# Kernel optimization log

Hardware: AMD Instinct MI355X
Metric: run time of the kernel (lower is better)

The kernel has to match this reference:

```python
import jax, jax.numpy as jnp
import numpy as np

B, P, ENC, DEC, ATT, EMB, V, MAXLEN = 64, 196, 2048, 1024, 1024, 1024, 10000, 20


def setup_inputs() -> dict:
    key = jax.random.key(0)
    ks = jax.random.split(key, 20)
    s = 0.02
    inp = {
        'encoder_out': jax.random.normal(ks[0], (B, 14, 14, ENC), jnp.float32),
        'encoded_captions': jax.random.randint(ks[1], (B, MAXLEN), 0, V),
        'caption_lengths': jax.random.randint(ks[2], (B, 1), 2, MAXLEN + 1).at[0, 0].set(MAXLEN),
        # embedding
        'emb_table': jax.random.uniform(ks[3], (V, EMB), jnp.float32, -0.1, 0.1),
        # attention MLP (weight_norm Linear == plain Linear math)
        'We': jax.random.normal(ks[4], (ATT, ENC)) * s,
        'be': jnp.zeros((ATT,), jnp.float32),
        'Wd': jax.random.normal(ks[5], (ATT, DEC)) * s,
        'bd': jnp.zeros((ATT,), jnp.float32),
        'Wf': jax.random.normal(ks[6], (1, ATT)) * s,
        'bf': jnp.zeros((1,), jnp.float32),
        # top_down_attention LSTMCell: input = EMB+ENC+DEC
        'W_ih1': jax.random.normal(ks[7], (4 * DEC, EMB + ENC + DEC)) * s,
        'W_hh1': jax.random.normal(ks[8], (4 * DEC, DEC)) * s,
        'b_ih1': jnp.zeros((4 * DEC,), jnp.float32),
        'b_hh1': jnp.zeros((4 * DEC,), jnp.float32),
        # language_model LSTMCell: input = ENC+DEC
        'W_ih2': jax.random.normal(ks[9], (4 * DEC, ENC + DEC)) * s,
        'W_hh2': jax.random.normal(ks[10], (4 * DEC, DEC)) * s,
        'b_ih2': jnp.zeros((4 * DEC,), jnp.float32),
        'b_hh2': jnp.zeros((4 * DEC,), jnp.float32),
        # output heads
        'Wfc1': jax.random.normal(ks[11], (V, DEC)) * s,
        'bfc1': jnp.zeros((V,), jnp.float32),
        'Wfc': jax.random.uniform(ks[12], (V, DEC), jnp.float32, -0.1, 0.1),
        'bfc': jnp.zeros((V,), jnp.float32),
    }
    return inp


def _lstm_cell(x, h, c, Wih, Whh, bih, bhh):
    g = x @ Wih.T + bih + h @ Whh.T + bhh
    i, f, gg, o = jnp.split(g, 4, axis=-1)  # torch gate order: i, f, g, o
    c2 = jax.nn.sigmoid(f) * c + jax.nn.sigmoid(i) * jnp.tanh(gg)
    h2 = jax.nn.sigmoid(o) * jnp.tanh(c2)
    return h2, c2


def _decode(encoder_out, encoded_captions, caption_lengths, emb_table,
            We, be, Wd, bd, Wf, bf,
            W_ih1, W_hh1, b_ih1, b_hh1, W_ih2, W_hh2, b_ih2, b_hh2,
            Wfc1, bfc1, Wfc, bfc):
    b = encoder_out.shape[0]
    enc = encoder_out.reshape(b, -1, encoder_out.shape[-1])  # (B,P,ENC)
    enc_mean = enc.mean(axis=1)
    cl = caption_lengths.squeeze(1)
    sort_ind = jnp.argsort(-cl)
    cl = cl[sort_ind]
    enc = enc[sort_ind]
    enc_mean = enc_mean[sort_ind]
    caps = encoded_captions[sort_ind]
    dec_len = cl - 1  # (B,)
    embeds = emb_table[caps]  # (B,T,EMB)
    Tdec = caps.shape[1] - 1
    # precompute encoder attention projection (loop-invariant, same math)
    att1 = jnp.einsum('bpe,ae->bpa', enc, We) + be  # (B,P,ATT)

    def step(carry, t):
        h1, c1, h2, c2 = carry
        active = (t < dec_len)[:, None]  # (B,1)
        x1 = jnp.concatenate([h2, enc_mean, embeds[:, t, :]], axis=1)
        h1n, c1n = _lstm_cell(x1, h1, c1, W_ih1, W_hh1, b_ih1, b_hh1)
        h1n = jnp.where(active, h1n, h1)
        c1n = jnp.where(active, c1n, c1)
        # Bahdanau attention
        att2 = h1n @ Wd.T + bd  # (B,ATT)
        e = jnp.einsum('bpa,a->bp', jax.nn.relu(att1 + att2[:, None, :]), Wf[0]) + bf[0]
        alpha = jax.nn.softmax(e, axis=1)
        awe = jnp.einsum('bpe,bp->be', enc, alpha)
        preds1 = h1n @ Wfc1.T + bfc1  # dropout is identity at eval
        x2 = jnp.concatenate([awe, h1n], axis=1)
        h2n, c2n = _lstm_cell(x2, h2, c2, W_ih2, W_hh2, b_ih2, b_hh2)
        h2n = jnp.where(active, h2n, h2)
        c2n = jnp.where(active, c2n, c2)
        preds = h2n @ Wfc.T + bfc
        preds = jnp.where(active, preds, 0.0)
        preds1 = jnp.where(active, preds1, 0.0)
        return (h1n, c1n, h2n, c2n), (preds, preds1)

    z = jnp.zeros((b, DEC), jnp.float32)
    (_, _, _, _), (pr, pr1) = jax.lax.scan(step, (z, z, z, z), jnp.arange(Tdec))
    predictions = jnp.transpose(pr, (1, 0, 2))  # (B,Tdec,V)
    predictions1 = jnp.transpose(pr1, (1, 0, 2))
    return predictions, predictions1, caps, dec_len, sort_ind


def reference(encoder_out, encoded_captions, caption_lengths, emb_table,
              We, be, Wd, bd, Wf, bf,
              W_ih1, W_hh1, b_ih1, b_hh1, W_ih2, W_hh2, b_ih2, b_hh2,
              Wfc1, bfc1, Wfc, bfc):
    return _decode(encoder_out, encoded_captions, caption_lengths, emb_table,
                   We, be, Wd, bd, Wf, bf,
                   W_ih1, W_hh1, b_ih1, b_hh1, W_ih2, W_hh2, b_ih2, b_hh2,
                   Wfc1, bfc1, Wfc, bfc)
```

## Files before the change

### kernel.cpp

```cpp
#include <hip/hip_runtime.h>
#include <cmath>

#define B_ 64
#define P_ 196
#define ENC_ 2048
#define DEC_ 1024
#define V_ 10000
#define MAXLEN_ 20
#define TDEC_ 19

typedef __attribute__((ext_vector_type(8))) short bf16x8;
typedef __attribute__((ext_vector_type(4))) float f32x4;


__device__ __align__(16) short g_encb[(size_t)12544 * 2048];
__device__ __align__(16) short g_encbt[(size_t)12544 * 2048];
__device__ __align__(16) short g_att1[(size_t)12544 * 1024];
__device__ __align__(16) short g_Wp1t[(size_t)4096 * 2048];
__device__ __align__(16) short g_Wemt[(size_t)4096 * 2048];
__device__ __align__(16) short g_Wembt[(size_t)4096 * 1024];
__device__ __align__(16) short g_Wc2t[(size_t)4096 * 4096];
__device__ __align__(16) short g_Webt[(size_t)1024 * 2048];
__device__ __align__(16) short g_Wdt[(size_t)1024 * 1024];
__device__ __align__(16) short g_Wfc1t[(size_t)10000 * 1024];
__device__ __align__(16) short g_Wfct[(size_t)10000 * 1024];
__device__ __align__(16) short g_xs1[(size_t)20 * 64 * 2048];
__device__ __align__(16) short g_xemb[(size_t)19 * 64 * 1024];
__device__ __align__(16) short g_xc2[(size_t)20 * 64 * 4096];
__device__ __align__(16) short g_em[64 * 2048];
__device__ __align__(16) float g_preemb[(size_t)19 * 64 * 4096];
__device__ __align__(16) float g_preem[64 * 4096];
__device__ __align__(16) float g_part[(size_t)16 * 64 * 4096];
__device__ __align__(16) float g_att2p[(size_t)8 * 64 * 1024];
__device__ __align__(16) float g_e[64 * P_];
__device__ __align__(16) float g_c1[64 * 1024];
__device__ __align__(16) float g_c2[64 * 1024];
__device__ int g_ibuf[64 + 64 + 64 * MAXLEN_];

__device__ __forceinline__ short f2b(float f) {
  unsigned u = __float_as_uint(f);
  u += 0x7FFFu + ((u >> 16) & 1u);
  return (short)(u >> 16);
}
__device__ __forceinline__ float b2f(short s) {
  return __uint_as_float(((unsigned)(unsigned short)s) << 16);
}

__global__ void k_sort(const int* __restrict__ cl_in, const int* __restrict__ caps_in,
                       int* __restrict__ sind, int* __restrict__ declen, int* __restrict__ caps_s,
                       float* __restrict__ out_caps, float* __restrict__ out_declen,
                       float* __restrict__ out_sind) {
  int i = threadIdx.x;
  __shared__ int cl[B_];
  cl[i] = cl_in[i];
  __syncthreads();
  int my = cl[i], pos = 0;
  for (int j = 0; j < B_; ++j) {
    int cj = cl[j];
    if (cj > my || (cj == my && j < i)) pos++;
  }
  sind[pos] = i;
  __syncthreads();
  int sb = sind[i];
  int dl = cl[sb] - 1;
  declen[i] = dl;
  out_declen[i] = (float)dl;
  out_sind[i] = (float)sb;
  for (int t = 0; t < MAXLEN_; ++t) {
    int v = caps_in[sb * MAXLEN_ + t];
    caps_s[i * MAXLEN_ + t] = v;
    out_caps[i * MAXLEN_ + t] = (float)v;
  }
}

__global__ __launch_bounds__(256) void k_encprep(const float* __restrict__ enc,
                                                 const int* __restrict__ sind,
                                                 short* __restrict__ encb,
                                                 short* __restrict__ encbt) {
  int mg = blockIdx.x;
  int b = mg / P_, p = mg - b * P_;
  int tid = threadIdx.x;
  const float* src = enc + ((size_t)sind[b] * P_ + p) * ENC_ + tid * 8;
  float4 a = *(const float4*)src;
  float4 c = *(const float4*)(src + 4);
  bf16x8 v;
  v[0] = f2b(a.x); v[1] = f2b(a.y); v[2] = f2b(a.z); v[3] = f2b(a.w);
  v[4] = f2b(c.x); v[5] = f2b(c.y); v[6] = f2b(c.z); v[7] = f2b(c.w);
  *(bf16x8*)(encb + (size_t)mg * ENC_ + tid * 8) = v;
  size_t off = (((size_t)(mg >> 4) * 64 + (tid >> 2)) << 9) +
               (((mg & 15) | ((tid & 3) << 4)) << 3);
  *(bf16x8*)(encbt + off) = v;
}

__global__ __launch_bounds__(64) void k_encmeanb(const short* __restrict__ encb,
                                                 short* __restrict__ em) {
  int b = blockIdx.x;
  int col0 = blockIdx.y * 512 + threadIdx.x * 8;
  const short* src = encb + (size_t)b * P_ * ENC_ + col0;
  float acc[8] = {};
  for (int p = 0; p < P_; ++p) {
    bf16x8 v = *(const bf16x8*)(src + (size_t)p * ENC_);
#pragma unroll
    for (int j = 0; j < 8; ++j) acc[j] += b2f(v[j]);
  }
#pragma unroll
  for (int j = 0; j < 8; ++j) em[b * 2048 + col0 + j] = f2b(acc[j] * (1.0f / 196.0f));
}

__global__ __launch_bounds__(256) void k_prefill(const float* __restrict__ emb,
                                                 const int* __restrict__ caps_s,
                                                 short* __restrict__ xemb) {
  int t = blockIdx.x, b = blockIdx.y, tid = threadIdx.x;
  short* xr = xemb + ((size_t)t * 64 + b) * 1024;
  int cap = caps_s[b * MAXLEN_ + t];
  int j = tid * 4;
  float4 v = *(const float4*)(emb + (size_t)cap * 1024 + j);
  short4 o;
  o.x = f2b(v.x); o.y = f2b(v.y); o.z = f2b(v.z); o.w = f2b(v.w);
  *(short4*)(xr + j) = o;
}

__global__ void k_f2bts(const float* __restrict__ src, int Kstride, int c0, int ncols,
                        short* __restrict__ dst, int Ktot, int koff) {
  int idx = blockIdx.x * 256 + threadIdx.x;
  int kc = ncols >> 3;
  int r = idx / kc, k8 = (idx - r * kc) << 3;
  const float* s = src + (size_t)r * Kstride + c0 + k8;
  float4 a = *(const float4*)s;
  float4 c = *(const float4*)(s + 4);
  bf16x8 v;
  v[0] = f2b(a.x); v[1] = f2b(a.y); v[2] = f2b(a.z); v[3] = f2b(a.w);
  v[4] = f2b(c.x); v[5] = f2b(c.y); v[6] = f2b(c.z); v[7] = f2b(c.w);
  int kg = koff + k8;
  size_t off = (((size_t)(r >> 4) * (Ktot >> 5) + (kg >> 5)) << 9) +
               (((r & 15) | (((kg >> 3) & 3) << 4)) << 3);
  *(bf16x8*)(dst + off) = v;
}

__global__ __launch_bounds__(512) void k_att1_t(const short* __restrict__ At,
                                                const short* __restrict__ Wt,
                                                const float* __restrict__ be,
                                                short* __restrict__ Cb) {
  int wg = blockIdx.x;
  wg = (wg & 7) * 49 + (wg >> 3);
  int bx = wg >> 2, by = wg & 3;
  int wave = threadIdx.x >> 6, lane = threadIdx.x & 63;
  int mt0 = bx * 8 + (wave >> 2) * 4;
  int nt0 = by * 16 + (wave & 3) * 4;
  f32x4 acc[4][4] = {};
  const short* Ab = At + ((size_t)mt0 * 64 << 9) + lane * 8;
  const short* Wb = Wt + ((size_t)nt0 * 64 << 9) + lane * 8;
  for (int kt = 0; kt < 64; ++kt) {
    bf16x8 a[4], b[4];
#pragma unroll
    for (int i = 0; i < 4; ++i) a[i] = *(const bf16x8*)(Ab + (((size_t)i * 64 + kt) << 9));
#pragma unroll
    for (int j = 0; j < 4; ++j) b[j] = *(const bf16x8*)(Wb + (((size_t)j * 64 + kt) << 9));
#pragma unroll
    for (int i = 0; i < 4; ++i)
#pragma unroll
      for (int j = 0; j < 4; ++j)
        acc[i][j] = __builtin_amdgcn_mfma_f32_16x16x32_bf16(a[i], b[j], acc[i][j], 0, 0, 0);
  }
  int rr = (lane >> 4) * 4, cc = lane & 15;
  int m0 = mt0 * 16, n0 = nt0 * 16;
#pragma unroll
  for (int i = 0; i < 4; ++i)
#pragma unroll
    for (int j = 0; j < 4; ++j) {
      int n = n0 + j * 16 + cc;
      float bn = be[n];
#pragma unroll
      for (int r = 0; r < 4; ++r) {
        int m = m0 + i * 16 + rr + r;
        Cb[(size_t)m * 1024 + n] = f2b(acc[i][j][r] + bn);
      }
    }
}

__global__ __launch_bounds__(256) void k_skinny_t(const short* __restrict__ A, int lda,
                                                  const short* __restrict__ Wt, int ldw,
                                                  int N, int kchunk, float* __restrict__ part) {
  int wave = threadIdx.x >> 6, lane = threadIdx.x & 63;
  int n0 = blockIdx.x * 128 + wave * 32;
  int kb = blockIdx.y * kchunk;
  int lr = lane & 15, lk = (lane >> 4) * 8;
  int ntk = ldw >> 5;
  int nt0 = n0 >> 4;
  f32x4 acc[4][2] = {};
  const short* Ab = A + (size_t)lr * lda + kb + lk;
  const short* Wb0 = Wt + (((size_t)nt0 * ntk + (kb >> 5)) << 9) + lane * 8;
  const short* Wb1 = Wt + (((size_t)(nt0 + 1) * ntk + (kb >> 5)) << 9) + lane * 8;
  int nkt = kchunk >> 5;
  for (int kt = 0; kt < nkt; ++kt) {
    bf16x8 a[4], b0, b1;
#pragma unroll
    for (int i = 0; i < 4; ++i) a[i] = *(const bf16x8*)(Ab + (size_t)i * 16 * lda + kt * 32);
    b0 = *(const bf16x8*)(Wb0 + ((size_t)kt << 9));
    b1 = *(const bf16x8*)(Wb1 + ((size_t)kt << 9));
#pragma unroll
    for (int i = 0; i < 4; ++i) {
      acc[i][0] = __builtin_amdgcn_mfma_f32_16x16x32_bf16(a[i], b0, acc[i][0], 0, 0, 0);
      acc[i][1] = __builtin_amdgcn_mfma_f32_16x16x32_bf16(a[i], b1, acc[i][1], 0, 0, 0);
    }
  }
  float* po = part + (size_t)blockIdx.y * 64 * N;
  int rr = (lane >> 4) * 4, cc = lane & 15;
#pragma unroll
  for (int i = 0; i < 4; ++i)
#pragma unroll
    for (int j = 0; j < 2; ++j) {
      int n = n0 + j * 16 + cc;
#pragma unroll
      for (int r = 0; r < 4; ++r) {
        int m = i * 16 + rr + r;
        po[(size_t)m * N + n] = acc[i][j][r];
      }
    }
}

__global__ void k_sumn(const float* __restrict__ part, int nsplit, float* __restrict__ dst) {
  int idx = blockIdx.x * 256 + threadIdx.x;
  float s = 0.0f;
  for (int q = 0; q < nsplit; ++q) s += part[(size_t)q * 64 * 4096 + idx];
  dst[idx] = s;
}

__global__ __launch_bounds__(256) void k_mid_emb4(const short* __restrict__ xemb,
                                                  const short* __restrict__ Wt,
                                                  float* __restrict__ preemb) {
  int wg = blockIdx.x;
  wg = (wg & 7) * 38 + (wg >> 3);
  int t = wg % 19;
  int nch = wg / 19;
  const short* A = xemb + (size_t)t * 64 * 1024;
  int wave = threadIdx.x >> 6, lane = threadIdx.x & 63;
  int nt0 = nch * 16 + wave * 4;
  int lr = lane & 15, lk = (lane >> 4) * 8;
  f32x4 acc[4][4] = {};
  const short* Ab = A + (size_t)lr * 1024 + lk;
  const short* Wb[4];
#pragma unroll
  for (int j = 0; j < 4; ++j) Wb[j] = Wt + ((size_t)(nt0 + j) * 32 << 9) + lane * 8;
  for (int kt = 0; kt < 32; ++kt) {
    bf16x8 a[4], b[4];
#pragma unroll
    for (int j = 0; j < 4; ++j) b[j] = *(const bf16x8*)(Wb[j] + ((size_t)kt << 9));
#pragma unroll
    for (int i = 0; i < 4; ++i) a[i] = *(const bf16x8*)(Ab + (size_t)i * 16 * 1024 + kt * 32);
#pragma unroll
    for (int i = 0; i < 4; ++i)
#pragma unroll
      for (int j = 0; j < 4; ++j)
        acc[i][j] = __builtin_amdgcn_mfma_f32_16x16x32_bf16(a[i], b[j], acc[i][j], 0, 0, 0);
  }
  float* po = preemb + (size_t)t * 64 * 4096;
  int rr = (lane >> 4) * 4, cc = lane & 15;
#pragma unroll
  for (int i = 0; i < 4; ++i)
#pragma unroll
    for (int j = 0; j < 4; ++j) {
      int n = (nt0 + j) * 16 + cc;
#pragma unroll
      for (int r = 0; r < 4; ++r) {
        int m = i * 16 + rr + r;
        po[(size_t)m * 4096 + n] = acc[i][j][r];
      }
    }
}

__global__ void k_gates(const float* __restrict__ part, int nsplit,
                        const float* __restrict__ pre, const float* __restrict__ pre2,
                        const float* __restrict__ bih, const float* __restrict__ bhh,
                        float* __restrict__ c,
                        const short* __restrict__ hold, int ldo,
                        short* __restrict__ dst1, int ld1,
                        short* __restrict__ dst2, int ld2,
                        const int* __restrict__ declen, int t) {
  int idx = blockIdx.x * 256 + threadIdx.x;
  int b = idx >> 10, j = idx & 1023;
  const float* pb = part + (size_t)b * 4096;
  float gi = bih[j] + bhh[j];
  float gf = bih[1024 + j] + bhh[1024 + j];
  float gg = bih[2048 + j] + bhh[2048 + j];
  float go = bih[3072 + j] + bhh[3072 + j];
  if (pre) {
    const float* pp = pre + (size_t)b * 4096;
    gi += pp[j]; gf += pp[j + 1024]; gg += pp[j + 2048]; go += pp[j + 3072];
  }
  if (pre2) {
    const float* pp = pre2 + (size_t)b * 4096;
    gi += pp[j]; gf += pp[j + 1024]; gg += pp[j + 2048]; go += pp[j + 3072];
  }
  for (int s = 0; s < nsplit; ++s) {
    const float* p = pb + (size_t)s * 64 * 4096;
    gi += p[j]; gf += p[j + 1024]; gg += p[j + 2048]; go += p[j + 3072];
  }
  float si = 1.0f / (1.0f + expf(-gi));
  float sf = 1.0f / (1.0f + expf(-gf));
  float so = 1.0f / (1.0f + expf(-go));
  float cn = sf * c[idx] + si * tanhf(gg);
  float hn = so * tanhf(cn);
  short hb;
  if (t < declen[b]) {
    c[idx] = cn;
    hb = f2b(hn);
  } else {
    hb = hold[b * ldo + j];
  }
  dst1[b * ld1 + j] = hb;
  dst2[b * ld2 + j] = hb;
}

__global__ __launch_bounds__(256) void k_e(const short* __restrict__ att1,
                                           const float* __restrict__ att2p,
                                           const float* __restrict__ bd,
                                           const float* __restrict__ Wf,
                                           const float* __restrict__ bf,
                                           float* __restrict__ e) {
  __shared__ float a2[1024];
  int b = blockIdx.x / 49, pq = blockIdx.x % 49;
  for (int i = threadIdx.x; i < 1024; i += 256) {
    float s = bd[i];
#pragma unroll
    for (int q = 0; q < 4; ++q) s += att2p[q * 65536 + b * 1024 + i];
    a2[i] = s;
  }
  __syncthreads();
  int wave = threadIdx.x >> 6, lane = threadIdx.x & 63;
  int p = pq * 4 + wave;
  const short* a1 = att1 + ((size_t)(b * P_ + p)) * 1024;
  float s = 0.0f;
#pragma unroll
  for (int h = 0; h < 2; ++h) {
    int k0 = lane * 8 + h * 512;
    bf16x8 v = *(const bf16x8*)(a1 + k0);
#pragma unroll
    for (int j = 0; j < 8; ++j) s += Wf[k0 + j] * fmaxf(b2f(v[j]) + a2[k0 + j], 0.0f);
  }
#pragma unroll
  for (int off = 32; off; off >>= 1) s += __shfl_down(s, off);
  if (lane == 0) e[b * P_ + p] = s + bf[0];
}

__global__ __launch_bounds__(256) void k_sawe(const float* __restrict__ e,
                                              const short* __restrict__ encb,
                                              short* __restrict__ xc2t) {
  int b = blockIdx.x, ch = blockIdx.y;
  __shared__ float al[P_];
  __shared__ float red[8][256];
  int tid = threadIdx.x;
  if (tid < 64) {
    float vals[4];
    float mx = -1e30f;
#pragma unroll
    for (int q = 0; q < 4; ++q) {
      int p = tid + q * 64;
      vals[q] = (p < P_) ? e[b * P_ + p] : -1e30f;
      mx = fmaxf(mx, vals[q]);
    }
#pragma unroll
    for (int off = 32; off; off >>= 1) mx = fmaxf(mx, __shfl_xor(mx, off));
    float sum = 0.0f;
#pragma unroll
    for (int q = 0; q < 4; ++q) {
      int p = tid + q * 64;
      vals[q] = (p < P_) ? expf(vals[q] - mx) : 0.0f;
      sum += vals[q];
    }
#pragma unroll
    for (int off = 32; off; off >>= 1) sum += __shfl_xor(sum, off);
    float inv = 1.0f / sum;
#pragma unroll
    for (int q = 0; q < 4; ++q) {
      int p = tid + q * 64;
      if (p < P_) al[p] = vals[q] * inv;
    }
  }
  __syncthreads();
  int pg = tid >> 5, cg = tid & 31;
  int col = ch * 256 + cg * 8;
  const short* src = encb + (size_t)b * P_ * ENC_ + col;
  float acc[8] = {};
  for (int p = pg; p < P_; p += 8) {
    bf16x8 v = *(const bf16x8*)(src + (size_t)p * ENC_);
    float ap = al[p];
#pragma unroll
    for (int j = 0; j < 8; ++j) acc[j] += ap * b2f(v[j]);
  }
#pragma unroll
  for (int j = 0; j < 8; ++j) red[pg][cg * 8 + j] = acc[j];
  __syncthreads();
  float s = 0.0f;
#pragma unroll
  for (int g = 0; g < 8; ++g) s += red[g][tid];
  xc2t[b * 4096 + ch * 256 + tid] = f2b(s);
}

__global__ __launch_bounds__(256) void k_head4(const short* __restrict__ Aall,
                                               const short* __restrict__ Wt,
                                               const float* __restrict__ bias,
                                               float* __restrict__ outp,
                                               const int* __restrict__ declen) {
  int wg = blockIdx.x;
  wg = (wg & 7) * 95 + (wg >> 3);
  int t = wg % 19;
  int nch = wg / 19;
  const short* A = Aall + (size_t)t * (64 * 4096);
  int wave = threadIdx.x >> 6, lane = threadIdx.x & 63;
  int nt0 = nch * 16 + wave * 4;
  int lr = lane & 15, lk = (lane >> 4) * 8;
  f32x4 acc[4][4] = {};
  const short* Ab = A + (size_t)lr * 4096 + lk;
  const short* Wb[4];
  bool ok[4];
#pragma unroll
  for (int j = 0; j < 4; ++j) {
    ok[j] = (nt0 + j) < (V_ >> 4);
    Wb[j] = Wt + ((size_t)(ok[j] ? nt0 + j : 0) * 32 << 9) + lane * 8;
  }
  for (int kt = 0; kt < 32; ++kt) {
    bf16x8 a[4], b[4];
#pragma unroll
    for (int j = 0; j < 4; ++j) b[j] = *(const bf16x8*)(Wb[j] + ((size_t)kt << 9));
#pragma unroll
    for (int i = 0; i < 4; ++i) a[i] = *(const bf16x8*)(Ab + (size_t)i * 16 * 4096 + kt * 32);
#pragma unroll
    for (int i = 0; i < 4; ++i)
#pragma unroll
      for (int j = 0; j < 4; ++j)
        acc[i][j] = __builtin_amdgcn_mfma_f32_16x16x32_bf16(a[i], b[j], acc[i][j], 0, 0, 0);
  }
  int rr = (lane >> 4) * 4, cc = lane & 15;
#pragma unroll
  for (int j = 0; j < 4; ++j) {
    if (!ok[j]) continue;
    int n = (nt0 + j) * 16 + cc;
    float bn = bias[n];
#pragma unroll
    for (int i = 0; i < 4; ++i) {
#pragma unroll
      for (int r = 0; r < 4; ++r) {
        int b = i * 16 + rr + r;
        float val = acc[i][j][r] + bn;
        outp[((size_t)b * TDEC_ + t) * V_ + n] = (t < declen[b]) ? val : 0.0f;
      }
    }
  }
}

extern "C" void kernel_launch(void* const* d_in, const int* in_sizes, int n_in,
                              void* d_out, int out_size, void* d_ws, size_t ws_size,
                              hipStream_t stream) {
  (void)in_sizes; (void)n_in; (void)d_ws; (void)ws_size; (void)out_size;
  const float* enc  = (const float*)d_in[0];
  const int*   caps = (const int*)d_in[1];
  const int*   cl   = (const int*)d_in[2];
  const float* emb  = (const float*)d_in[3];
  const float* We   = (const float*)d_in[4];
  const float* be   = (const float*)d_in[5];
  const float* Wd   = (const float*)d_in[6];
  const float* bd   = (const float*)d_in[7];
  const float* Wf   = (const float*)d_in[8];
  const float* bf   = (const float*)d_in[9];
  const float* Wih1 = (const float*)d_in[10];
  const float* Whh1 = (const float*)d_in[11];
  const float* bih1 = (const float*)d_in[12];
  const float* bhh1 = (const float*)d_in[13];
  const float* Wih2 = (const float*)d_in[14];
  const float* Whh2 = (const float*)d_in[15];
  const float* bih2 = (const float*)d_in[16];
  const float* bhh2 = (const float*)d_in[17];
  const float* Wfc1 = (const float*)d_in[18];
  const float* bfc1 = (const float*)d_in[19];
  const float* Wfc  = (const float*)d_in[20];
  const float* bfc  = (const float*)d_in[21];
  float* out = (float*)d_out;

  short *encb, *encbt, *att1, *Wp1t, *Wemt, *Wembt, *Wc2t, *Webt, *Wdt, *Wfc1t, *Wfct;
  short *xs1, *xemb, *xc2, *em;
  float *preemb, *preem, *part, *att2p, *e, *c1, *c2;
  int* ib;
  hipGetSymbolAddress((void**)&encb, HIP_SYMBOL(g_encb));
  hipGetSymbolAddress((void**)&encbt, HIP_SYMBOL(g_encbt));
  hipGetSymbolAddress((void**)&att1, HIP_SYMBOL(g_att1));
  hipGetSymbolAddress((void**)&Wp1t, HIP_SYMBOL(g_Wp1t));
  hipGetSymbolAddress((void**)&Wemt, HIP_SYMBOL(g_Wemt));
  hipGetSymbolAddress((void**)&Wembt, HIP_SYMBOL(g_Wembt));
  hipGetSymbolAddress((void**)&Wc2t, HIP_SYMBOL(g_Wc2t));
  hipGetSymbolAddress((void**)&Webt, HIP_SYMBOL(g_Webt));
  hipGetSymbolAddress((void**)&Wdt, HIP_SYMBOL(g_Wdt));
  hipGetSymbolAddress((void**)&Wfc1t, HIP_SYMBOL(g_Wfc1t));
  hipGetSymbolAddress((void**)&Wfct, HIP_SYMBOL(g_Wfct));
  hipGetSymbolAddress((void**)&xs1, HIP_SYMBOL(g_xs1));
  hipGetSymbolAddress((void**)&xemb, HIP_SYMBOL(g_xemb));
  hipGetSymbolAddress((void**)&xc2, HIP_SYMBOL(g_xc2));
  hipGetSymbolAddress((void**)&em, HIP_SYMBOL(g_em));
  hipGetSymbolAddress((void**)&preemb, HIP_SYMBOL(g_preemb));
  hipGetSymbolAddress((void**)&preem, HIP_SYMBOL(g_preem));
  hipGetSymbolAddress((void**)&part, HIP_SYMBOL(g_part));
  hipGetSymbolAddress((void**)&att2p, HIP_SYMBOL(g_att2p));
  hipGetSymbolAddress((void**)&e, HIP_SYMBOL(g_e));
  hipGetSymbolAddress((void**)&c1, HIP_SYMBOL(g_c1));
  hipGetSymbolAddress((void**)&c2, HIP_SYMBOL(g_c2));
  hipGetSymbolAddress((void**)&ib, HIP_SYMBOL(g_ibuf));
  int* sind = ib;
  int* declen = ib + 64;
  int* caps_s = ib + 128;

  float* out_preds  = out;
  float* out_preds1 = out + (size_t)B_ * TDEC_ * V_;
  float* out_caps   = out + 2ull * B_ * TDEC_ * V_;
  float* out_declen = out_caps + B_ * MAXLEN_;
  float* out_sind   = out_declen + B_;

  k_sort<<<1, 64, 0, stream>>>(cl, caps, sind, declen, caps_s, out_caps, out_declen, out_sind);
  hipMemsetAsync(c1, 0, 64 * 1024 * sizeof(float), stream);
  hipMemsetAsync(c2, 0, 64 * 1024 * sizeof(float), stream);
  hipMemsetAsync(xs1, 0, (size_t)64 * 2048 * sizeof(short), stream);
  hipMemsetAsync(xc2, 0, (size_t)64 * 4096 * sizeof(short), stream);
  k_encprep<<<12544, 256, 0, stream>>>(enc, sind, encb, encbt);
  k_encmeanb<<<dim3(64, 4), 64, 0, stream>>>(encb, em);
  k_prefill<<<dim3(19, 64), 256, 0, stream>>>(emb, caps_s, xemb);
  k_f2bts<<<2048, 256, 0, stream>>>(Wih1, 4096, 0, 1024, Wp1t, 2048, 0);
  k_f2bts<<<2048, 256, 0, stream>>>(Whh1, 1024, 0, 1024, Wp1t, 2048, 1024);
  k_f2bts<<<4096, 256, 0, stream>>>(Wih1, 4096, 1024, 2048, Wemt, 2048, 0);
  k_f2bts<<<2048, 256, 0, stream>>>(Wih1, 4096, 3072, 1024, Wembt, 1024, 0);
  k_f2bts<<<6144, 256, 0, stream>>>(Wih2, 3072, 0, 3072, Wc2t, 4096, 0);
  k_f2bts<<<2048, 256, 0, stream>>>(Whh2, 1024, 0, 1024, Wc2t, 4096, 3072);
  k_f2bts<<<1024, 256, 0, stream>>>(We, 2048, 0, 2048, Webt, 2048, 0);
  k_f2bts<<<512, 256, 0, stream>>>(Wd, 1024, 0, 1024, Wdt, 1024, 0);
  k_f2bts<<<5000, 256, 0, stream>>>(Wfc1, 1024, 0, 1024, Wfc1t, 1024, 0);
  k_f2bts<<<5000, 256, 0, stream>>>(Wfc, 1024, 0, 1024, Wfct, 1024, 0);
  k_att1_t<<<392, 512, 0, stream>>>(encbt, Webt, be, att1);
  k_skinny_t<<<dim3(32, 4), 256, 0, stream>>>(em, 2048, Wemt, 2048, 4096, 512, part);
  k_sumn<<<1024, 256, 0, stream>>>(part, 4, preem);
  k_mid_emb4<<<304, 256, 0, stream>>>(xemb, Wembt, preemb);

  for (int t = 0; t < TDEC_; ++t) {
    short* s1t = xs1 + (size_t)t * 64 * 2048;
    short* s1n = xs1 + (size_t)(t + 1) * 64 * 2048;
    short* x2t = xc2 + (size_t)t * 64 * 4096;
    short* x2n = xc2 + (size_t)(t + 1) * 64 * 4096;
    k_skinny_t<<<dim3(32, 8), 256, 0, stream>>>(s1t, 2048, Wp1t, 2048, 4096, 256, part);
    k_gates<<<256, 256, 0, stream>>>(part, 8, preemb + (size_t)t * 64 * 4096, preem,
                                     bih1, bhh1, c1, s1t + 1024, 2048,
                                     s1n + 1024, 2048, x2t + 2048, 4096, declen, t);
    k_skinny_t<<<dim3(8, 4), 256, 0, stream>>>(x2t + 2048, 4096, Wdt, 1024, 1024, 256, att2p);
    k_e<<<3136, 256, 0, stream>>>(att1, att2p, bd, Wf, bf, e);
    k_sawe<<<dim3(64, 8), 256, 0, stream>>>(e, encb, x2t);
    k_skinny_t<<<dim3(32, 8), 256, 0, stream>>>(x2t, 4096, Wc2t, 4096, 4096, 512, part);
    k_gates<<<256, 256, 0, stream>>>(part, 8, nullptr, nullptr, bih2, bhh2, c2, s1t, 2048,
                                     s1n, 2048, x2n + 3072, 4096, declen, t);
  }
  k_head4<<<760, 256, 0, stream>>>(xc2 + 2048, Wfc1t, bfc1, out_preds1, declen);
  k_head4<<<760, 256, 0, stream>>>(xc2 + 64 * 4096 + 3072, Wfct, bfc, out_preds, declen);
}
```

Measured before the change: 1.833 ms.

## Batch weight conversions into one launch, coarsen attention-score kernel, drop att1 swizzle

Ten separate fp32-to-bf16 weight conversion launches are merged into one kernel that picks its job from a block-offset table passed by value, cutting launch overhead. The per-step attention-score kernel now has each wave handle four pixels, so a block covers 16, which reduces block count and repeats the 1024-element att2 reduction into shared memory fewer times. The att1 GEMM drops its XCD-aware block index swizzle in favour of a plain 2D grid, which may change L2 locality.

```diff
diff --git a/kernel.cpp b/kernel.cpp
--- a/kernel.cpp
+++ b/kernel.cpp
@@ -120,33 +120,46 @@
   *(short4*)(xr + j) = o;
 }
 
-__global__ void k_f2bts(const float* __restrict__ src, int Kstride, int c0, int ncols,
-                        short* __restrict__ dst, int Ktot, int koff) {
-  int idx = blockIdx.x * 256 + threadIdx.x;
-  int kc = ncols >> 3;
+struct F2BJobs {
+  const float* src[10];
+  short* dst[10];
+  int kstride[10];
+  int c0[10];
+  int ncols[10];
+  int ktot[10];
+  int koff[10];
+  int base[11];
+};
+
+__global__ __launch_bounds__(256) void k_f2bt_all(F2BJobs jb) {
+  int bg = blockIdx.x;
+  int j = 0;
+#pragma unroll
+  for (int q = 1; q < 10; ++q)
+    if (bg >= jb.base[q]) j = q;
+  int idx = (bg - jb.base[j]) * 256 + threadIdx.x;
+  int kc = jb.ncols[j] >> 3;
   int r = idx / kc, k8 = (idx - r * kc) << 3;
-  const float* s = src + (size_t)r * Kstride + c0 + k8;
+  const float* s = jb.src[j] + (size_t)r * jb.kstride[j] + jb.c0[j] + k8;
   float4 a = *(const float4*)s;
   float4 c = *(const float4*)(s + 4);
   bf16x8 v;
   v[0] = f2b(a.x); v[1] = f2b(a.y); v[2] = f2b(a.z); v[3] = f2b(a.w);
   v[4] = f2b(c.x); v[5] = f2b(c.y); v[6] = f2b(c.z); v[7] = f2b(c.w);
-  int kg = koff + k8;
+  int kg = jb.koff[j] + k8;
+  int Ktot = jb.ktot[j];
   size_t off = (((size_t)(r >> 4) * (Ktot >> 5) + (kg >> 5)) << 9) +
                (((r & 15) | (((kg >> 3) & 3) << 4)) << 3);
-  *(bf16x8*)(dst + off) = v;
+  *(bf16x8*)(jb.dst[j] + off) = v;
 }
 
 __global__ __launch_bounds__(512) void k_att1_t(const short* __restrict__ At,
                                                 const short* __restrict__ Wt,
                                                 const float* __restrict__ be,
                                                 short* __restrict__ Cb) {
-  int wg = blockIdx.x;
-  wg = (wg & 7) * 49 + (wg >> 3);
-  int bx = wg >> 2, by = wg & 3;
   int wave = threadIdx.x >> 6, lane = threadIdx.x & 63;
-  int mt0 = bx * 8 + (wave >> 2) * 4;
-  int nt0 = by * 16 + (wave & 3) * 4;
+  int mt0 = blockIdx.x * 8 + (wave >> 2) * 4;
+  int nt0 = blockIdx.y * 16 + (wave & 3) * 4;
   f32x4 acc[4][4] = {};
   const short* Ab = At + ((size_t)mt0 * 64 << 9) + lane * 8;
   const short* Wb = Wt + ((size_t)nt0 * 64 << 9) + lane * 8;
@@ -319,7 +332,7 @@
                                            const float* __restrict__ bf,
                                            float* __restrict__ e) {
   __shared__ float a2[1024];
-  int b = blockIdx.x / 49, pq = blockIdx.x % 49;
+  int b = blockIdx.x / 13, pq = blockIdx.x % 13;
   for (int i = threadIdx.x; i < 1024; i += 256) {
     float s = bd[i];
 #pragma unroll
@@ -328,19 +341,23 @@
   }
   __syncthreads();
   int wave = threadIdx.x >> 6, lane = threadIdx.x & 63;
-  int p = pq * 4 + wave;
-  const short* a1 = att1 + ((size_t)(b * P_ + p)) * 1024;
-  float s = 0.0f;
-#pragma unroll
-  for (int h = 0; h < 2; ++h) {
-    int k0 = lane * 8 + h * 512;
-    bf16x8 v = *(const bf16x8*)(a1 + k0);
-#pragma unroll
-    for (int j = 0; j < 8; ++j) s += Wf[k0 + j] * fmaxf(b2f(v[j]) + a2[k0 + j], 0.0f);
-  }
-#pragma unroll
-  for (int off = 32; off; off >>= 1) s += __shfl_down(s, off);
-  if (lane == 0) e[b * P_ + p] = s + bf[0];
+#pragma unroll
+  for (int i = 0; i < 4; ++i) {
+    int p = pq * 16 + wave * 4 + i;
+    if (p >= P_) break;
+    const short* a1 = att1 + ((size_t)(b * P_ + p)) * 1024;
+    float s = 0.0f;
+#pragma unroll
+    for (int h = 0; h < 2; ++h) {
+      int k0 = lane * 8 + h * 512;
+      bf16x8 v = *(const bf16x8*)(a1 + k0);
+#pragma unroll
+      for (int j = 0; j < 8; ++j) s += Wf[k0 + j] * fmaxf(b2f(v[j]) + a2[k0 + j], 0.0f);
+    }
+#pragma unroll
+    for (int off = 32; off; off >>= 1) s += __shfl_down(s, off);
+    if (lane == 0) e[b * P_ + p] = s + bf[0];
+  }
 }
 
 __global__ __launch_bounds__(256) void k_sawe(const float* __restrict__ e,
@@ -522,17 +539,27 @@
   k_encprep<<<12544, 256, 0, stream>>>(enc, sind, encb, encbt);
   k_encmeanb<<<dim3(64, 4), 64, 0, stream>>>(encb, em);
   k_prefill<<<dim3(19, 64), 256, 0, stream>>>(emb, caps_s, xemb);
-  k_f2bts<<<2048, 256, 0, stream>>>(Wih1, 4096, 0, 1024, Wp1t, 2048, 0);
-  k_f2bts<<<2048, 256, 0, stream>>>(Whh1, 1024, 0, 1024, Wp1t, 2048, 1024);
-  k_f2bts<<<4096, 256, 0, stream>>>(Wih1, 4096, 1024, 2048, Wemt, 2048, 0);
-  k_f2bts<<<2048, 256, 0, stream>>>(Wih1, 4096, 3072, 1024, Wembt, 1024, 0);
-  k_f2bts<<<6144, 256, 0, stream>>>(Wih2, 3072, 0, 3072, Wc2t, 4096, 0);
-  k_f2bts<<<2048, 256, 0, stream>>>(Whh2, 1024, 0, 1024, Wc2t, 4096, 3072);
-  k_f2bts<<<1024, 256, 0, stream>>>(We, 2048, 0, 2048, Webt, 2048, 0);
-  k_f2bts<<<512, 256, 0, stream>>>(Wd, 1024, 0, 1024, Wdt, 1024, 0);
-  k_f2bts<<<5000, 256, 0, stream>>>(Wfc1, 1024, 0, 1024, Wfc1t, 1024, 0);
-  k_f2bts<<<5000, 256, 0, stream>>>(Wfc, 1024, 0, 1024, Wfct, 1024, 0);
-  k_att1_t<<<392, 512, 0, stream>>>(encbt, Webt, be, att1);
+  {
+    F2BJobs jb;
+    const float* srcs[10] = {Wih1, Whh1, Wih1, Wih1, Wih2, Whh2, We, Wd, Wfc1, Wfc};
+    short* dsts[10] = {Wp1t, Wp1t, Wemt, Wembt, Wc2t, Wc2t, Webt, Wdt, Wfc1t, Wfct};
+    int kstride[10] = {4096, 1024, 4096, 4096, 3072, 1024, 2048, 1024, 1024, 1024};
+    int c0s[10]     = {0, 0, 1024, 3072, 0, 0, 0, 0, 0, 0};
+    int ncols[10]   = {1024, 1024, 2048, 1024, 3072, 1024, 2048, 1024, 1024, 1024};
+    int ktots[10]   = {2048, 2048, 2048, 1024, 4096, 4096, 2048, 1024, 1024, 1024};
+    int koffs[10]   = {0, 1024, 0, 0, 0, 3072, 0, 0, 0, 0};
+    int nblk[10]    = {2048, 2048, 4096, 2048, 6144, 2048, 1024, 512, 5000, 5000};
+    int cum = 0;
+    for (int q = 0; q < 10; ++q) {
+      jb.src[q] = srcs[q]; jb.dst[q] = dsts[q];
+      jb.kstride[q] = kstride[q]; jb.c0[q] = c0s[q]; jb.ncols[q] = ncols[q];
+      jb.ktot[q] = ktots[q]; jb.koff[q] = koffs[q];
+      jb.base[q] = cum; cum += nblk[q];
+    }
+    jb.base[10] = cum;
+    k_f2bt_all<<<cum, 256, 0, stream>>>(jb);
+  }
+  k_att1_t<<<dim3(98, 4), 512, 0, stream>>>(encbt, Webt, be, att1);
   k_skinny_t<<<dim3(32, 4), 256, 0, stream>>>(em, 2048, Wemt, 2048, 4096, 512, part);
   k_sumn<<<1024, 256, 0, stream>>>(part, 4, preem);
   k_mid_emb4<<<304, 256, 0, stream>>>(xemb, Wembt, preemb);
@@ -547,7 +574,7 @@
                                      bih1, bhh1, c1, s1t + 1024, 2048,
                                      s1n + 1024, 2048, x2t + 2048, 4096, declen, t);
     k_skinny_t<<<dim3(8, 4), 256, 0, stream>>>(x2t + 2048, 4096, Wdt, 1024, 1024, 256, att2p);
-    k_e<<<3136, 256, 0, stream>>>(att1, att2p, bd, Wf, bf, e);
+    k_e<<<832, 256, 0, stream>>>(att1, att2p, bd, Wf, bf, e);
     k_sawe<<<dim3(64, 8), 256, 0, stream>>>(e, encb, x2t);
     k_skinny_t<<<dim3(32, 8), 256, 0, stream>>>(x2t, 4096, Wc2t, 4096, 4096, 512, part);
     k_gates<<<256, 256, 0, stream>>>(part, 8, nullptr, nullptr, bih2, bhh2, c2, s1t, 2048,
```

New measurement: 1.754 ms. 4.3% less time.
